# Kernel optimization log

Measured on AMD Instinct MI355X. Metric: run time of the kernel, lower is better.

## Reference

```python
import jax, jax.numpy as jnp
import numpy as np
import math


def _dfrtmtrx(Npts, a):
    # Faithful to torch dfrtmtrx: Evec = I, so einsum('ij,jk,ni->nk', f, I, I) == f,
    # i.e. F = sqrt(N) * diag(exp(-1j*pi/2 * a * l)) with l = [0..N-2, N-1+even].
    even = 1 - Npts % 2
    l = jnp.arange(Npts).at[-1].add(even)            # last entry is N-1+even
    diag = jnp.exp((-1j) * (math.pi / 2) * a * l)     # complex64 when a is float32
    return (Npts ** 0.5) * jnp.diag(diag)             # [Npts, Npts] complex64


def setup_inputs() -> dict:
    key = jax.random.key(0)
    k1, k2 = jax.random.split(key)
    x = jax.random.normal(k1, (8, 64, 256, 256), dtype=jnp.float32)
    order = jax.random.normal(k2, (1,), dtype=jnp.float32)  # nn.Parameter(torch.randn(1))
    return {"x": x, "order": order}


def reference(x, order):
    N, C, H, W = x.shape
    a = order[0]
    Fh = _dfrtmtrx(H, a)  # [H, H] complex64
    Fw = _dfrtmtrx(W, a)  # [W, W] complex64
    xs = jnp.fft.fftshift(x, axes=(2, 3)).astype(jnp.complex64)
    # torch broadcasts h_test/w_test over (N, C) via repeat_interleave; plain
    # broadcasting in the einsum is the same math without materializing copies.
    out = jnp.einsum('hk,nckw->nchw', Fh, xs)   # left transform along H
    out = jnp.einsum('nchw,wk->nchk', out, Fw)  # right transform along W
    return jnp.fft.fftshift(out, axes=(2, 3))
```

## Files before the change

kernel.cpp:

```cpp
#include <hip/hip_runtime.h>


typedef float f32x2 __attribute__((ext_vector_type(2)));
typedef float f32x4 __attribute__((ext_vector_type(4)));

constexpr int HW    = 256;
constexpr int BLOCK = 256;
constexpr int KIT   = 8;

__global__ __launch_bounds__(BLOCK) void frft_diag_kernel(
    const float* __restrict__ x,
    const float* __restrict__ order,
    float* __restrict__ out,
    int interleaved,
    int nvec4)
{
    __shared__ alignas(16) f32x2 tbl[HW];

    const int t = threadIdx.x;
    {
        const int idx = t ^ 128;
        const double l = (idx == 255) ? 256.0 : (double)idx;
        const double theta = 1.5707963267948966 * (double)order[0] * l;
        double s, c;
        sincos(theta, &s, &c);
        tbl[t] = (f32x2){(float)(16.0 * c), (float)(16.0 * s)};
    }
    __syncthreads();

    const int wbase = (t & 63) << 2;
    const f32x4 twA = *reinterpret_cast<const f32x4*>(&tbl[wbase]);
    const f32x4 twB = *reinterpret_cast<const f32x4*>(&tbl[wbase + 2]);

    const int base = blockIdx.x * (BLOCK * KIT) + t;

#pragma unroll
    for (int k = 0; k < KIT; ++k) {
        const int p = base + k * BLOCK;
        if (p >= nvec4) continue;

        const f32x4 xv = ((const f32x4*)x)[p];
        const f32x2 th = tbl[(p >> 6) & (HW - 1)];

        const float pr0 = th.x * twA.x - th.y * twA.y;
        const float pr1 = th.x * twA.z - th.y * twA.w;
        const float pr2 = th.x * twB.x - th.y * twB.y;
        const float pr3 = th.x * twB.z - th.y * twB.w;

        if (interleaved) {
            const float pi0 = th.x * twA.y + th.y * twA.x;
            const float pi1 = th.x * twA.w + th.y * twA.z;
            const float pi2 = th.x * twB.y + th.y * twB.x;
            const float pi3 = th.x * twB.w + th.y * twB.z;
            f32x4 oA = { xv.x * pr0, -xv.x * pi0, xv.y * pr1, -xv.y * pi1 };
            f32x4 oB = { xv.z * pr2, -xv.z * pi2, xv.w * pr3, -xv.w * pi3 };
            __builtin_nontemporal_store(oA, &((f32x4*)out)[2 * p]);
            __builtin_nontemporal_store(oB, &((f32x4*)out)[2 * p + 1]);
        } else {
            f32x4 o = { xv.x * pr0, xv.y * pr1, xv.z * pr2, xv.w * pr3 };
            __builtin_nontemporal_store(o, &((f32x4*)out)[p]);
        }
    }
}

extern "C" void kernel_launch(void* const* d_in, const int* in_sizes, int n_in,
                              void* d_out, int out_size, void* d_ws, size_t ws_size,
                              hipStream_t stream) {
    const float* x     = (const float*)d_in[0];
    const float* order = (const float*)d_in[1];
    float* out = (float*)d_out;

    const int total = in_sizes[0];
    const int nvec4 = total / 4;
    const int interleaved = (out_size >= 2 * total) ? 1 : 0;

    const int per_block = BLOCK * KIT;
    const int grid = (nvec4 + per_block - 1) / per_block;
    frft_diag_kernel<<<grid, BLOCK, 0, stream>>>(x, order, out, interleaved, nvec4);
}
```

Before: 232.8 us.

## Precompute twiddle table in a prologue kernel, batch loads, drop nontemporal stores

```diff
diff --git a/kernel.cpp b/kernel.cpp
--- a/kernel.cpp
+++ b/kernel.cpp
@@ -8,23 +8,36 @@
 constexpr int BLOCK = 256;
 constexpr int KIT   = 8;
 
+__device__ __forceinline__ f32x2 diag_entry(const float* order, int t) {
+    const int idx = t ^ 128;
+    const double l = (idx == 255) ? 256.0 : (double)idx;
+    const double theta = 1.5707963267948966 * (double)order[0] * l;
+    double s, c;
+    sincos(theta, &s, &c);
+    return (f32x2){(float)(16.0 * c), (float)(16.0 * s)};
+}
+
+__global__ __launch_bounds__(BLOCK) void frft_table_kernel(
+    const float* __restrict__ order, float* __restrict__ tbl_g)
+{
+    const int t = threadIdx.x;
+    ((f32x2*)tbl_g)[t] = diag_entry(order, t);
+}
+
 __global__ __launch_bounds__(BLOCK) void frft_diag_kernel(
     const float* __restrict__ x,
     const float* __restrict__ order,
+    const float* __restrict__ tbl_g,
     float* __restrict__ out,
     int interleaved,
     int nvec4)
 {
     __shared__ alignas(16) f32x2 tbl[HW];
-
     const int t = threadIdx.x;
-    {
-        const int idx = t ^ 128;
-        const double l = (idx == 255) ? 256.0 : (double)idx;
-        const double theta = 1.5707963267948966 * (double)order[0] * l;
-        double s, c;
-        sincos(theta, &s, &c);
-        tbl[t] = (f32x2){(float)(16.0 * c), (float)(16.0 * s)};
+    if (tbl_g) {
+        tbl[t] = ((const f32x2*)tbl_g)[t];
+    } else {
+        tbl[t] = diag_entry(order, t);
     }
     __syncthreads();
 
@@ -34,19 +47,36 @@
 
     const int base = blockIdx.x * (BLOCK * KIT) + t;
 
+    if (!interleaved && base + (KIT - 1) * BLOCK < nvec4) {
+        f32x4 xv[KIT];
+#pragma unroll
+        for (int k = 0; k < KIT; ++k)
+            xv[k] = ((const f32x4*)x)[base + k * BLOCK];
+
+#pragma unroll
+        for (int k = 0; k < KIT; ++k) {
+            const int p = base + k * BLOCK;
+            const f32x2 th = tbl[(p >> 6) & (HW - 1)];
+            const float pr0 = th.x * twA.x - th.y * twA.y;
+            const float pr1 = th.x * twA.z - th.y * twA.w;
+            const float pr2 = th.x * twB.x - th.y * twB.y;
+            const float pr3 = th.x * twB.z - th.y * twB.w;
+            f32x4 o = { xv[k].x * pr0, xv[k].y * pr1, xv[k].z * pr2, xv[k].w * pr3 };
+            ((f32x4*)out)[p] = o;
+        }
+        return;
+    }
+
 #pragma unroll
     for (int k = 0; k < KIT; ++k) {
         const int p = base + k * BLOCK;
         if (p >= nvec4) continue;
-
         const f32x4 xv = ((const f32x4*)x)[p];
         const f32x2 th = tbl[(p >> 6) & (HW - 1)];
-
         const float pr0 = th.x * twA.x - th.y * twA.y;
         const float pr1 = th.x * twA.z - th.y * twA.w;
         const float pr2 = th.x * twB.x - th.y * twB.y;
         const float pr3 = th.x * twB.z - th.y * twB.w;
-
         if (interleaved) {
             const float pi0 = th.x * twA.y + th.y * twA.x;
             const float pi1 = th.x * twA.w + th.y * twA.z;
@@ -54,11 +84,11 @@
             const float pi3 = th.x * twB.w + th.y * twB.z;
             f32x4 oA = { xv.x * pr0, -xv.x * pi0, xv.y * pr1, -xv.y * pi1 };
             f32x4 oB = { xv.z * pr2, -xv.z * pi2, xv.w * pr3, -xv.w * pi3 };
-            __builtin_nontemporal_store(oA, &((f32x4*)out)[2 * p]);
-            __builtin_nontemporal_store(oB, &((f32x4*)out)[2 * p + 1]);
+            ((f32x4*)out)[2 * p]     = oA;
+            ((f32x4*)out)[2 * p + 1] = oB;
         } else {
             f32x4 o = { xv.x * pr0, xv.y * pr1, xv.z * pr2, xv.w * pr3 };
-            __builtin_nontemporal_store(o, &((f32x4*)out)[p]);
+            ((f32x4*)out)[p] = o;
         }
     }
 }
@@ -74,7 +104,14 @@
     const int nvec4 = total / 4;
     const int interleaved = (out_size >= 2 * total) ? 1 : 0;
 
+    float* tbl_g = nullptr;
+    if (d_ws && ws_size >= HW * sizeof(f32x2)) {
+        tbl_g = (float*)d_ws;
+        frft_table_kernel<<<1, BLOCK, 0, stream>>>(order, tbl_g);
+    }
+
     const int per_block = BLOCK * KIT;
     const int grid = (nvec4 + per_block - 1) / per_block;
-    frft_diag_kernel<<<grid, BLOCK, 0, stream>>>(x, order, out, interleaved, nvec4);
+    frft_diag_kernel<<<grid, BLOCK, 0, stream>>>(x, order, tbl_g, out,
+                                                 interleaved, nvec4);
 }
```

Result: no change. 231.5 us (-0.6%).

## Issue input loads before table setup and use two grid-strided vectors per thread

Applied to the files above, without the earlier changes.

```diff
diff --git a/kernel.cpp b/kernel.cpp
--- a/kernel.cpp
+++ b/kernel.cpp
@@ -6,7 +6,7 @@
 
 constexpr int HW    = 256;
 constexpr int BLOCK = 256;
-constexpr int KIT   = 8;
+constexpr int KIT   = 2;
 
 __global__ __launch_bounds__(BLOCK) void frft_diag_kernel(
     const float* __restrict__ x,
@@ -18,6 +18,15 @@
     __shared__ alignas(16) f32x2 tbl[HW];
 
     const int t = threadIdx.x;
+    const int stride = gridDim.x * BLOCK;
+    const int p0 = blockIdx.x * BLOCK + t;
+    const int p1 = p0 + stride;
+
+    f32x4 xv0 = {0, 0, 0, 0}, xv1 = {0, 0, 0, 0};
+    const bool l0 = (p0 < nvec4), l1 = (p1 < nvec4);
+    if (l0) xv0 = ((const f32x4*)x)[p0];
+    if (l1) xv1 = ((const f32x4*)x)[p1];
+
     {
         const int idx = t ^ 128;
         const double l = (idx == 255) ? 256.0 : (double)idx;
@@ -32,33 +41,47 @@
     const f32x4 twA = *reinterpret_cast<const f32x4*>(&tbl[wbase]);
     const f32x4 twB = *reinterpret_cast<const f32x4*>(&tbl[wbase + 2]);
 
-    const int base = blockIdx.x * (BLOCK * KIT) + t;
+    const f32x2 th0 = tbl[(p0 >> 6) & (HW - 1)];
+    const f32x2 th1 = tbl[(p1 >> 6) & (HW - 1)];
 
-#pragma unroll
-    for (int k = 0; k < KIT; ++k) {
-        const int p = base + k * BLOCK;
-        if (p >= nvec4) continue;
+    const float a0 = th0.x * twA.x - th0.y * twA.y;
+    const float a1 = th0.x * twA.z - th0.y * twA.w;
+    const float a2 = th0.x * twB.x - th0.y * twB.y;
+    const float a3 = th0.x * twB.z - th0.y * twB.w;
+    const float b0 = th1.x * twA.x - th1.y * twA.y;
+    const float b1 = th1.x * twA.z - th1.y * twA.w;
+    const float b2 = th1.x * twB.x - th1.y * twB.y;
+    const float b3 = th1.x * twB.z - th1.y * twB.w;
 
-        const f32x4 xv = ((const f32x4*)x)[p];
-        const f32x2 th = tbl[(p >> 6) & (HW - 1)];
-
-        const float pr0 = th.x * twA.x - th.y * twA.y;
-        const float pr1 = th.x * twA.z - th.y * twA.w;
-        const float pr2 = th.x * twB.x - th.y * twB.y;
-        const float pr3 = th.x * twB.z - th.y * twB.w;
-
-        if (interleaved) {
-            const float pi0 = th.x * twA.y + th.y * twA.x;
-            const float pi1 = th.x * twA.w + th.y * twA.z;
-            const float pi2 = th.x * twB.y + th.y * twB.x;
-            const float pi3 = th.x * twB.w + th.y * twB.z;
-            f32x4 oA = { xv.x * pr0, -xv.x * pi0, xv.y * pr1, -xv.y * pi1 };
-            f32x4 oB = { xv.z * pr2, -xv.z * pi2, xv.w * pr3, -xv.w * pi3 };
-            __builtin_nontemporal_store(oA, &((f32x4*)out)[2 * p]);
-            __builtin_nontemporal_store(oB, &((f32x4*)out)[2 * p + 1]);
-        } else {
-            f32x4 o = { xv.x * pr0, xv.y * pr1, xv.z * pr2, xv.w * pr3 };
-            __builtin_nontemporal_store(o, &((f32x4*)out)[p]);
+    if (!interleaved) {
+        if (l0) {
+            f32x4 o0 = { xv0.x * a0, xv0.y * a1, xv0.z * a2, xv0.w * a3 };
+            ((f32x4*)out)[p0] = o0;
+        }
+        if (l1) {
+            f32x4 o1 = { xv1.x * b0, xv1.y * b1, xv1.z * b2, xv1.w * b3 };
+            ((f32x4*)out)[p1] = o1;
+        }
+    } else {
+        const float ai0 = th0.x * twA.y + th0.y * twA.x;
+        const float ai1 = th0.x * twA.w + th0.y * twA.z;
+        const float ai2 = th0.x * twB.y + th0.y * twB.x;
+        const float ai3 = th0.x * twB.w + th0.y * twB.z;
+        const float bi0 = th1.x * twA.y + th1.y * twA.x;
+        const float bi1 = th1.x * twA.w + th1.y * twA.z;
+        const float bi2 = th1.x * twB.y + th1.y * twB.x;
+        const float bi3 = th1.x * twB.w + th1.y * twB.z;
+        if (l0) {
+            f32x4 oA = { xv0.x * a0, -xv0.x * ai0, xv0.y * a1, -xv0.y * ai1 };
+            f32x4 oB = { xv0.z * a2, -xv0.z * ai2, xv0.w * a3, -xv0.w * ai3 };
+            ((f32x4*)out)[2 * p0]     = oA;
+            ((f32x4*)out)[2 * p0 + 1] = oB;
+        }
+        if (l1) {
+            f32x4 oA = { xv1.x * b0, -xv1.x * bi0, xv1.y * b1, -xv1.y * bi1 };
+            f32x4 oB = { xv1.z * b2, -xv1.z * bi2, xv1.w * b3, -xv1.w * bi3 };
+            ((f32x4*)out)[2 * p1]     = oA;
+            ((f32x4*)out)[2 * p1 + 1] = oB;
         }
     }
 }
```

After: 234.5 us. Within noise of the previous version (+0.7%).
